# Kernel tuning notes

Hardware: AMD Instinct MI355X
Metric: run time of the kernel (lower is better)

## Reference

```python
import jax, jax.numpy as jnp
import numpy as np

B, T, EMB = 2, 2048, 1024
H, D = 16, 64          # num_heads, head_dim; hidden = H*D = 1024
SCALE = D ** (-0.5)


def setup_inputs() -> dict:
    key = jax.random.key(0)
    k1, k2, k3, k4, k5 = jax.random.split(key, 5)
    return {
        "x":    jax.random.normal(k1, (B, T, EMB), dtype=jnp.float32),
        "Wqkv": jax.random.normal(k2, (EMB, 3 * H * D), dtype=jnp.float32) * (EMB ** -0.5),
        "bqkv": jax.random.normal(k3, (3 * H * D,), dtype=jnp.float32) * 0.02,
        "Wout": jax.random.normal(k4, (H * D, EMB), dtype=jnp.float32) * ((H * D) ** -0.5),
        "bout": jax.random.normal(k5, (EMB,), dtype=jnp.float32) * 0.02,
    }


def reference(x, Wqkv, bqkv, Wout, bout):
    b, t, _ = x.shape
    qkv = x @ Wqkv + bqkv                                   # [b, t, 3*H*D]
    q, k, v = jnp.split(qkv, 3, axis=-1)
    split_heads = lambda a: a.reshape(b, t, H, D).transpose(0, 2, 1, 3)  # [b,h,t,d]
    q, k, v = split_heads(q), split_heads(k), split_heads(v)

    scores = jnp.einsum('bhid,bhjd->bhij', q, k) * SCALE    # [b,h,t,t]
    causal = jnp.tril(jnp.ones((t, t), dtype=bool))         # lower-triangular mask
    scores = jnp.where(causal, scores, -jnp.inf)
    attn = jax.nn.softmax(scores, axis=-1)                  # dropout: eval mode (identity)

    out = jnp.einsum('bhij,bhjd->bhid', attn, v)            # [b,h,t,d]
    out = out.transpose(0, 2, 1, 3).reshape(b, t, H * D)    # [b,t,H*D]
    return out @ Wout + bout                                # [b,t,EMB]
```

## Files before the change

kernel.cpp:

```cpp
#include <hip/hip_runtime.h>
#include <hip/hip_bf16.h>

typedef __bf16 bf16x8 __attribute__((ext_vector_type(8)));
typedef float f32x4 __attribute__((ext_vector_type(4)));
typedef float f32x16 __attribute__((ext_vector_type(16)));
typedef unsigned int uint32x4v __attribute__((ext_vector_type(4)));

#define B_ 2
#define T_ 2048
#define EMB_ 1024
#define H_ 16
#define D_ 64
#define M_ (B_ * T_)
#define NQKV_ (3 * H_ * D_)

#define QSCALE 0.18033688011112042f

#define GPTR(p) ((const __attribute__((address_space(1))) unsigned int*)(p))
#define LPTR(p) ((__attribute__((address_space(3))) unsigned int*)(p))

__device__ __forceinline__ unsigned pk2(float a, float b) {
    unsigned short ua = __builtin_bit_cast(unsigned short, (__bf16)a);
    unsigned short ub = __builtin_bit_cast(unsigned short, (__bf16)b);
    return (unsigned)ua | ((unsigned)ub << 16);
}

__global__ void cast_bf16_k(const float* __restrict__ in, __bf16* __restrict__ out) {
    int i = (blockIdx.x * blockDim.x + threadIdx.x) * 8;
    float4 a = *reinterpret_cast<const float4*>(in + i);
    float4 b = *reinterpret_cast<const float4*>(in + i + 4);
    bf16x8 o;
    o[0] = (__bf16)a.x; o[1] = (__bf16)a.y; o[2] = (__bf16)a.z; o[3] = (__bf16)a.w;
    o[4] = (__bf16)b.x; o[5] = (__bf16)b.y; o[6] = (__bf16)b.z; o[7] = (__bf16)b.w;
    *reinterpret_cast<bf16x8*>(out + i) = o;
}

__global__ void transpose_cast_k(const float* __restrict__ in, __bf16* __restrict__ out,
                                 int K, int N) {
    __shared__ float tile[32][33];
    int bx = blockIdx.x;
    int by = blockIdx.y;
    int tx = threadIdx.x, ty = threadIdx.y;
    for (int j = 0; j < 32; j += 8)
        tile[ty + j][tx] = in[(size_t)(by * 32 + ty + j) * N + bx * 32 + tx];
    __syncthreads();
    for (int j = 0; j < 32; j += 8)
        out[(size_t)(bx * 32 + ty + j) * K + by * 32 + tx] = (__bf16)tile[tx][ty + j];
}

#define BM 128
#define BN 128
#define BK 64

template <int EPI>
__global__ __launch_bounds__(256, 2) void gemm_bf16_k(
    const __bf16* __restrict__ A, const __bf16* __restrict__ Bt,
    const float* __restrict__ bias, float* __restrict__ outF,
    __bf16* __restrict__ Qg, __bf16* __restrict__ Kg, __bf16* __restrict__ Vtg,
    int Mdim, int Ndim, int Kdim) {
    __shared__ __bf16 As[2][BM * BK];
    __shared__ __bf16 Bs[2][BN * BK];
    const int tid = threadIdx.x;
    const int lane = tid & 63;
    const int w = tid >> 6;
    const int wr = w >> 1, wc = w & 1;
    const int row0 = blockIdx.y * BM;
    const int col0 = blockIdx.x * BN;
    const int lr = lane & 15;
    const int lg = lane >> 4;

    f32x4 acc[4][4] = {};

    const int srow = 32 * w;
    const int lrow = lane >> 3;
    const int scc = ((lane & 7) ^ (lrow & 7)) * 8;

    auto STAGE = [&](int t, int bufi) {
        const int k0 = t * BK;
        #pragma unroll
        for (int i = 0; i < 4; ++i) {
            int r0 = srow + 8 * i;
            int row = r0 + lrow;
            __builtin_amdgcn_global_load_lds(
                GPTR(A + (size_t)(row0 + row) * Kdim + k0 + scc), LPTR(&As[bufi][r0 * BK]), 16, 0, 0);
            __builtin_amdgcn_global_load_lds(
                GPTR(Bt + (size_t)(col0 + row) * Kdim + k0 + scc), LPTR(&Bs[bufi][r0 * BK]), 16, 0, 0);
        }
    };

    const int nk = Kdim / BK;
    STAGE(0, 0);
    __syncthreads();
    for (int t = 0; t < nk; ++t) {
        if (t + 1 < nk) STAGE(t + 1, (t + 1) & 1);
        const __bf16* __restrict__ Ab = As[t & 1];
        const __bf16* __restrict__ Bb = Bs[t & 1];
        #pragma unroll
        for (int kk = 0; kk < BK; kk += 32) {
            bf16x8 af[4], bfr[4];
            #pragma unroll
            for (int mt = 0; mt < 4; ++mt) {
                int row = wr * 64 + mt * 16 + lr;
                int cc = ((kk / 8 + lg) ^ (row & 7)) * 8;
                af[mt] = *reinterpret_cast<const bf16x8*>(&Ab[row * BK + cc]);
            }
            #pragma unroll
            for (int nt = 0; nt < 4; ++nt) {
                int row = wc * 64 + nt * 16 + lr;
                int cc = ((kk / 8 + lg) ^ (row & 7)) * 8;
                bfr[nt] = *reinterpret_cast<const bf16x8*>(&Bb[row * BK + cc]);
            }
            #pragma unroll
            for (int mt = 0; mt < 4; ++mt)
                #pragma unroll
                for (int nt = 0; nt < 4; ++nt)
                    acc[mt][nt] = __builtin_amdgcn_mfma_f32_16x16x32_bf16(
                        af[mt], bfr[nt], acc[mt][nt], 0, 0, 0);
        }
        __syncthreads();
    }

    #pragma unroll
    for (int mt = 0; mt < 4; ++mt)
        #pragma unroll
        for (int nt = 0; nt < 4; ++nt)
            #pragma unroll
            for (int r = 0; r < 4; ++r) {
                int row = row0 + wr * 64 + mt * 16 + lg * 4 + r;
                int col = col0 + wc * 64 + nt * 16 + lr;
                float v = acc[mt][nt][r] + bias[col];
                if (EPI == 0) {
                    outF[(size_t)row * Ndim + col] = v;
                } else {
                    int part = col >> 10;
                    int hh = (col >> 6) & 15;
                    int dd = col & 63;
                    int bb = row >> 11;
                    int tt = row & 2047;
                    size_t bh = (size_t)(bb * H_ + hh);
                    if (part == 0)
                        Qg[(bh * T_ + tt) * D_ + dd] = (__bf16)(v * QSCALE);
                    else if (part == 1)
                        Kg[(bh * T_ + tt) * D_ + dd] = (__bf16)v;
                    else
                        Vtg[(bh * D_ + dd) * T_ + tt] = (__bf16)v;
                }
            }
}

#define KVB 64
#define QBLK 64

template <bool MASK>
__device__ __forceinline__ void attn_tile(
    const bf16x8 (&qf)[4], const __bf16* __restrict__ Ksb, const __bf16* __restrict__ Vsb,
    f32x16& o0, f32x16& o1, float& m, float& lsum, int thr, int hi, int l31) {
    const int cb = l31 & 7;
    bf16x8 kf0[4], kf1[4];
    #pragma unroll
    for (int ks = 0; ks < 4; ++ks) {
        int c = ((2 * ks + hi) ^ cb) * 8;
        kf0[ks] = *reinterpret_cast<const bf16x8*>(&Ksb[l31 * 64 + c]);
        kf1[ks] = *reinterpret_cast<const bf16x8*>(&Ksb[(32 + l31) * 64 + c]);
    }
    f32x16 s0 = {}, s1 = {};
    __builtin_amdgcn_s_setprio(1);
    #pragma unroll
    for (int ks = 0; ks < 4; ++ks) {
        s0 = __builtin_amdgcn_mfma_f32_32x32x16_bf16(kf0[ks], qf[ks], s0, 0, 0, 0);
        s1 = __builtin_amdgcn_mfma_f32_32x32x16_bf16(kf1[ks], qf[ks], s1, 0, 0, 0);
    }
    __builtin_amdgcn_s_setprio(0);
    if (MASK) {
        #pragma unroll
        for (int r = 0; r < 16; ++r) {
            int c = (r & 3) + 8 * (r >> 2);
            if (c > thr) s0[r] = -1e30f;
            if (c + 32 > thr) s1[r] = -1e30f;
        }
    }
    float pmax = -1e30f;
    #pragma unroll
    for (int r = 0; r < 16; ++r) pmax = fmaxf(pmax, fmaxf(s0[r], s1[r]));
    pmax = fmaxf(pmax, __shfl_xor(pmax, 32, 64));
    if (__any(pmax > m + 8.f)) {
        float mnew = fmaxf(m, pmax);
        float corr = __builtin_exp2f(m - mnew);
        m = mnew;
        lsum *= corr;
        #pragma unroll
        for (int r = 0; r < 16; ++r) {
            int qsrc = (r & 3) + 8 * (r >> 2) + 4 * hi;
            float cbr = __shfl(corr, qsrc, 64);
            o0[r] *= cbr; o1[r] *= cbr;
        }
    }
    float ps = 0.f;
    #pragma unroll
    for (int r = 0; r < 16; ++r) {
        s0[r] = __builtin_exp2f(s0[r] - m);
        s1[r] = __builtin_exp2f(s1[r] - m);
        ps += s0[r] + s1[r];
    }
    ps += __shfl_xor(ps, 32, 64);
    lsum += ps;
    #pragma unroll
    for (int ks = 0; ks < 4; ++ks) {
        const int e = (ks & 1) * 8;
        unsigned w0, w1, w2, w3;
        if (ks < 2) {
            w0 = pk2(s0[e + 0], s0[e + 1]); w1 = pk2(s0[e + 2], s0[e + 3]);
            w2 = pk2(s0[e + 4], s0[e + 5]); w3 = pk2(s0[e + 6], s0[e + 7]);
        } else {
            w0 = pk2(s1[e + 0], s1[e + 1]); w1 = pk2(s1[e + 2], s1[e + 3]);
            w2 = pk2(s1[e + 4], s1[e + 5]); w3 = pk2(s1[e + 6], s1[e + 7]);
        }
        unsigned pw0 = __shfl_xor(w0, 32, 64);
        unsigned pw1 = __shfl_xor(w1, 32, 64);
        unsigned pw2 = __shfl_xor(w2, 32, 64);
        unsigned pw3 = __shfl_xor(w3, 32, 64);
        uint32x4v uf;
        uf.x = hi ? pw2 : w0;
        uf.y = hi ? pw3 : w1;
        uf.z = hi ? w2 : pw0;
        uf.w = hi ? w3 : pw1;
        bf16x8 pa = __builtin_bit_cast(bf16x8, uf);
        int c = ((2 * ks + hi) ^ cb) * 8;
        bf16x8 vf0 = *reinterpret_cast<const bf16x8*>(&Vsb[l31 * 64 + c]);
        bf16x8 vf1 = *reinterpret_cast<const bf16x8*>(&Vsb[(32 + l31) * 64 + c]);
        __builtin_amdgcn_s_setprio(1);
        o0 = __builtin_amdgcn_mfma_f32_32x32x16_bf16(pa, vf0, o0, 0, 0, 0);
        o1 = __builtin_amdgcn_mfma_f32_32x32x16_bf16(pa, vf1, o1, 0, 0, 0);
        __builtin_amdgcn_s_setprio(0);
    }
}

__global__ __launch_bounds__(128, 2) void attn_k(
    const __bf16* __restrict__ Qg, const __bf16* __restrict__ Kg,
    const __bf16* __restrict__ Vtg, __bf16* __restrict__ Og) {
    __shared__ __bf16 Ks[2][KVB * 64];
    __shared__ __bf16 Vs[2][64 * KVB];

    const int tid = threadIdx.x;
    const int lane = tid & 63;
    const int w = tid >> 6;
    const int l31 = lane & 31;
    const int hi = lane >> 5;
    const int bid = blockIdx.x;
    const int bh = bid & 31;
    const int idx = bid >> 5;
    const int qb = (idx < 16) ? (31 - idx) : (idx - 16);
    const int q0 = qb * QBLK;
    const int qw = q0 + w * 32;
    const int q_lane = qw + l31;
    const int ntile = qb + 1;
    const size_t baseQK = (size_t)bh * T_ * D_;
    const size_t baseVt = (size_t)bh * D_ * T_;

    const int lrow = lane >> 3;
    const int lc = lane & 7;

    auto STAGE = [&](int t, int bufi) {
        const int kv0 = t * KVB;
        #pragma unroll
        for (int i = 0; i < 4; ++i) {
            int r0 = i * 16 + w * 8;
            int row = r0 + lrow;
            int c = (lc ^ (row & 7)) * 8;
            __builtin_amdgcn_global_load_lds(
                GPTR(Kg + baseQK + (size_t)(kv0 + row) * D_ + c),
                LPTR(&Ks[bufi][r0 * 64]), 16, 0, 0);
            __builtin_amdgcn_global_load_lds(
                GPTR(Vtg + baseVt + (size_t)row * T_ + kv0 + c),
                LPTR(&Vs[bufi][r0 * 64]), 16, 0, 0);
        }
    };

    bf16x8 qf[4];
    #pragma unroll
    for (int ks = 0; ks < 4; ++ks)
        qf[ks] = *reinterpret_cast<const bf16x8*>(
            &Qg[baseQK + (size_t)q_lane * D_ + ks * 16 + hi * 8]);

    f32x16 o0 = {}, o1 = {};
    float m = -1e30f, lsum = 0.f;

    STAGE(0, 0);
    __syncthreads();
    for (int t = 0; t < ntile - 1; ++t) {
        STAGE(t + 1, (t + 1) & 1);
        attn_tile<false>(qf, Ks[t & 1], Vs[t & 1], o0, o1, m, lsum, 0, hi, l31);
        __syncthreads();
    }
    attn_tile<true>(qf, Ks[(ntile - 1) & 1], Vs[(ntile - 1) & 1],
                    o0, o1, m, lsum, q_lane - (ntile - 1) * KVB - 4 * hi, hi, l31);

    const int b = bh >> 4, h = bh & 15;
    float li = 1.0f / lsum;
    #pragma unroll
    for (int r = 0; r < 16; ++r) {
        int qsrc = (r & 3) + 8 * (r >> 2) + 4 * hi;
        float cbr = __shfl(li, qsrc, 64);
        int tt = qw + qsrc;
        size_t base = (size_t)(b * T_ + tt) * (H_ * D_) + h * D_;
        Og[base + l31]      = (__bf16)(o0[r] * cbr);
        Og[base + 32 + l31] = (__bf16)(o1[r] * cbr);
    }
}

extern "C" void kernel_launch(void* const* d_in, const int* in_sizes, int n_in,
                              void* d_out, int out_size, void* d_ws, size_t ws_size,
                              hipStream_t stream) {
    const float* x    = (const float*)d_in[0];
    const float* Wqkv = (const float*)d_in[1];
    const float* bqkv = (const float*)d_in[2];
    const float* Wout = (const float*)d_in[3];
    const float* bout = (const float*)d_in[4];
    float* outF = (float*)d_out;

    char* ws = (char*)d_ws;
    __bf16* xb     = (__bf16*)(ws);
    __bf16* WqkvT  = (__bf16*)(ws + 8388608);
    __bf16* WoutT  = (__bf16*)(ws + 14680064);
    __bf16* Qg     = (__bf16*)(ws + 16777216);
    __bf16* Kg     = (__bf16*)(ws + 25165824);
    __bf16* Vtg    = (__bf16*)(ws + 33554432);
    __bf16* Og     = (__bf16*)(ws + 41943040);

    cast_bf16_k<<<(M_ * EMB_) / (256 * 8), 256, 0, stream>>>(x, xb);
    transpose_cast_k<<<dim3(NQKV_ / 32, EMB_ / 32), dim3(32, 8), 0, stream>>>(Wqkv, WqkvT, EMB_, NQKV_);
    transpose_cast_k<<<dim3(EMB_ / 32, EMB_ / 32), dim3(32, 8), 0, stream>>>(Wout, WoutT, EMB_, EMB_);

    gemm_bf16_k<1><<<dim3(NQKV_ / BN, M_ / BM), 256, 0, stream>>>(
        xb, WqkvT, bqkv, nullptr, Qg, Kg, Vtg, M_, NQKV_, EMB_);

    attn_k<<<1024, 128, 0, stream>>>(Qg, Kg, Vtg, Og);

    gemm_bf16_k<0><<<dim3(EMB_ / BN, M_ / BM), 256, 0, stream>>>(
        Og, WoutT, bout, outF, nullptr, nullptr, nullptr, M_, EMB_, EMB_);
}
```

Baseline: 221.4 us.

## Run attention with one wave per 32-query block and drop block barriers

The attention kernel now launches 2048 single-wave blocks, each owning 32 query rows, in place of 1024 two-wave blocks. Because only one wave touches the shared K/V buffers, the __syncthreads calls are replaced by explicit s_waitcnt vmcnt waits on the async global-to-LDS loads. The softmax max and sum reductions become tree reductions, and the P-fragment exchange uses two lane shuffles instead of four. The cost is that K/V tiles are fetched separately for every 32 queries rather than shared across 64, which roughly doubles L2-to-LDS traffic and gives a less regular block schedule.

```diff
diff --git a/kernel.cpp b/kernel.cpp
--- a/kernel.cpp
+++ b/kernel.cpp
@@ -149,7 +149,6 @@
 }
 
 #define KVB 64
-#define QBLK 64
 
 template <bool MASK>
 __device__ __forceinline__ void attn_tile(
@@ -179,9 +178,14 @@
             if (c + 32 > thr) s1[r] = -1e30f;
         }
     }
-    float pmax = -1e30f;
-    #pragma unroll
-    for (int r = 0; r < 16; ++r) pmax = fmaxf(pmax, fmaxf(s0[r], s1[r]));
+    float m8[8];
+    #pragma unroll
+    for (int i = 0; i < 8; ++i)
+        m8[i] = fmaxf(fmaxf(s0[i], s0[i + 8]), fmaxf(s1[i], s1[i + 8]));
+    float m4[4];
+    #pragma unroll
+    for (int i = 0; i < 4; ++i) m4[i] = fmaxf(m8[i], m8[i + 4]);
+    float pmax = fmaxf(fmaxf(m4[0], m4[1]), fmaxf(m4[2], m4[3]));
     pmax = fmaxf(pmax, __shfl_xor(pmax, 32, 64));
     if (__any(pmax > m + 8.f)) {
         float mnew = fmaxf(m, pmax);
@@ -195,13 +199,19 @@
             o0[r] *= cbr; o1[r] *= cbr;
         }
     }
-    float ps = 0.f;
     #pragma unroll
     for (int r = 0; r < 16; ++r) {
         s0[r] = __builtin_exp2f(s0[r] - m);
         s1[r] = __builtin_exp2f(s1[r] - m);
-        ps += s0[r] + s1[r];
-    }
+    }
+    float a8[8];
+    #pragma unroll
+    for (int i = 0; i < 8; ++i)
+        a8[i] = (s0[i] + s0[i + 8]) + (s1[i] + s1[i + 8]);
+    float a4[4];
+    #pragma unroll
+    for (int i = 0; i < 4; ++i) a4[i] = a8[i] + a8[i + 4];
+    float ps = (a4[0] + a4[1]) + (a4[2] + a4[3]);
     ps += __shfl_xor(ps, 32, 64);
     lsum += ps;
     #pragma unroll
@@ -215,15 +225,15 @@
             w0 = pk2(s1[e + 0], s1[e + 1]); w1 = pk2(s1[e + 2], s1[e + 3]);
             w2 = pk2(s1[e + 4], s1[e + 5]); w3 = pk2(s1[e + 6], s1[e + 7]);
         }
-        unsigned pw0 = __shfl_xor(w0, 32, 64);
-        unsigned pw1 = __shfl_xor(w1, 32, 64);
-        unsigned pw2 = __shfl_xor(w2, 32, 64);
-        unsigned pw3 = __shfl_xor(w3, 32, 64);
+        unsigned X = hi ? w0 : w2;
+        unsigned Y = hi ? w1 : w3;
+        unsigned Xp = __shfl_xor(X, 32, 64);
+        unsigned Yp = __shfl_xor(Y, 32, 64);
         uint32x4v uf;
-        uf.x = hi ? pw2 : w0;
-        uf.y = hi ? pw3 : w1;
-        uf.z = hi ? w2 : pw0;
-        uf.w = hi ? w3 : pw1;
+        uf.x = hi ? Xp : w0;
+        uf.y = hi ? Yp : w1;
+        uf.z = hi ? w2 : Xp;
+        uf.w = hi ? w3 : Yp;
         bf16x8 pa = __builtin_bit_cast(bf16x8, uf);
         int c = ((2 * ks + hi) ^ cb) * 8;
         bf16x8 vf0 = *reinterpret_cast<const bf16x8*>(&Vsb[l31 * 64 + c]);
@@ -235,25 +245,21 @@
     }
 }
 
-__global__ __launch_bounds__(128, 2) void attn_k(
+__global__ __launch_bounds__(64, 1) void attn_k(
     const __bf16* __restrict__ Qg, const __bf16* __restrict__ Kg,
     const __bf16* __restrict__ Vtg, __bf16* __restrict__ Og) {
     __shared__ __bf16 Ks[2][KVB * 64];
     __shared__ __bf16 Vs[2][64 * KVB];
 
-    const int tid = threadIdx.x;
-    const int lane = tid & 63;
-    const int w = tid >> 6;
+    const int lane = threadIdx.x;
     const int l31 = lane & 31;
     const int hi = lane >> 5;
     const int bid = blockIdx.x;
     const int bh = bid & 31;
-    const int idx = bid >> 5;
-    const int qb = (idx < 16) ? (31 - idx) : (idx - 16);
-    const int q0 = qb * QBLK;
-    const int qw = q0 + w * 32;
-    const int q_lane = qw + l31;
-    const int ntile = qb + 1;
+    const int qt = 63 - (bid >> 5);
+    const int q0 = qt * 32;
+    const int q_lane = q0 + l31;
+    const int ntile = (qt >> 1) + 1;
     const size_t baseQK = (size_t)bh * T_ * D_;
     const size_t baseVt = (size_t)bh * D_ * T_;
 
@@ -263,8 +269,8 @@
     auto STAGE = [&](int t, int bufi) {
         const int kv0 = t * KVB;
         #pragma unroll
-        for (int i = 0; i < 4; ++i) {
-            int r0 = i * 16 + w * 8;
+        for (int i = 0; i < 8; ++i) {
+            int r0 = i * 8;
             int row = r0 + lrow;
             int c = (lc ^ (row & 7)) * 8;
             __builtin_amdgcn_global_load_lds(
@@ -286,14 +292,22 @@
     float m = -1e30f, lsum = 0.f;
 
     STAGE(0, 0);
-    __syncthreads();
-    for (int t = 0; t < ntile - 1; ++t) {
-        STAGE(t + 1, (t + 1) & 1);
-        attn_tile<false>(qf, Ks[t & 1], Vs[t & 1], o0, o1, m, lsum, 0, hi, l31);
-        __syncthreads();
-    }
-    attn_tile<true>(qf, Ks[(ntile - 1) & 1], Vs[(ntile - 1) & 1],
-                    o0, o1, m, lsum, q_lane - (ntile - 1) * KVB - 4 * hi, hi, l31);
+    for (int t = 0; t < ntile; ++t) {
+        const bool pf = (t + 1 < ntile);
+        if (pf) {
+            STAGE(t + 1, (t + 1) & 1);
+            asm volatile("s_waitcnt vmcnt(16)" ::: "memory");
+        } else {
+            asm volatile("s_waitcnt vmcnt(0)" ::: "memory");
+        }
+        __builtin_amdgcn_sched_barrier(0);
+        if (pf) {
+            attn_tile<false>(qf, Ks[t & 1], Vs[t & 1], o0, o1, m, lsum, 0, hi, l31);
+        } else {
+            attn_tile<true>(qf, Ks[t & 1], Vs[t & 1], o0, o1, m, lsum,
+                            q_lane - t * KVB - 4 * hi, hi, l31);
+        }
+    }
 
     const int b = bh >> 4, h = bh & 15;
     float li = 1.0f / lsum;
@@ -301,7 +315,7 @@
     for (int r = 0; r < 16; ++r) {
         int qsrc = (r & 3) + 8 * (r >> 2) + 4 * hi;
         float cbr = __shfl(li, qsrc, 64);
-        int tt = qw + qsrc;
+        int tt = q0 + qsrc;
         size_t base = (size_t)(b * T_ + tt) * (H_ * D_) + h * D_;
         Og[base + l31]      = (__bf16)(o0[r] * cbr);
         Og[base + 32 + l31] = (__bf16)(o1[r] * cbr);
@@ -334,7 +348,7 @@
     gemm_bf16_k<1><<<dim3(NQKV_ / BN, M_ / BM), 256, 0, stream>>>(
         xb, WqkvT, bqkv, nullptr, Qg, Kg, Vtg, M_, NQKV_, EMB_);
 
-    attn_k<<<1024, 128, 0, stream>>>(Qg, Kg, Vtg, Og);
+    attn_k<<<2048, 64, 0, stream>>>(Qg, Kg, Vtg, Og);
 
     gemm_bf16_k<0><<<dim3(EMB_ / BN, M_ / BM), 256, 0, stream>>>(
         Og, WoutT, bout, outF, nullptr, nullptr, nullptr, M_, EMB_, EMB_);
```

New measurement: 240.6 us. 1.09x slower.
